# Performance work log

Measured on AMD Instinct MI355X. Metric: run time of the kernel, lower is better.

The kernel has to match this reference:

```python
import jax, jax.numpy as jnp
import numpy as np

N, D, M, K = 4096, 512, 50000, 32
TEMP = 0.1          # config.temperature
LAMBDA_GEOM = 0.1   # config.lambda_geom
LAMBDA_COMP = 0.1   # config.lambda_comp


def _unit(v):
    return v / jnp.linalg.norm(v, axis=-1, keepdims=True)


def setup_inputs() -> dict:
    key = jax.random.key(0)
    kx, km, ka, kk, kw, kb = jax.random.split(key, 6)
    x = _unit(jax.random.normal(kx, (N, D), jnp.float32))
    mu = _unit(jax.random.normal(km, (M, D), jnp.float32))            # splat directions
    alpha = jax.random.uniform(ka, (M,), jnp.float32, 1.0, 20.0)      # concentrations
    kappa = jax.random.uniform(kk, (M,), jnp.float32, 0.0, 2.0)       # importances
    W_w = jax.random.normal(kw, (3,), jnp.float32) * 0.5              # Linear(3,1) weight
    W_b = jax.random.normal(kb, (), jnp.float32) * 0.1                # Linear(3,1) bias
    return {"x": x, "mu": mu, "alpha": alpha, "kappa": kappa, "W_w": W_w, "W_b": W_b}


def reference(x, mu, alpha, kappa, W_w, W_b):
    # --- kNN over splats (find_neighbors): cosine/dot similarity top-k ---
    sims = x @ mu.T                                   # [N, M]
    dots, idx = jax.lax.top_k(sims, K)                # [N, K] neighbor dot-products + indices

    # --- splat energy: weighted logsumexp over neighbors ---
    n_alpha = alpha[idx]                              # [N, K]
    n_kappa = kappa[idx]                              # [N, K]
    imp = jnp.clip(n_kappa, 1e-4)
    weights = imp / imp.sum(axis=-1, keepdims=True)
    exponent = n_alpha * (dots - 1.0) / TEMP
    weighted = exponent + jnp.log(jnp.clip(weights, 1e-8))
    e_splat = -jax.nn.logsumexp(weighted, axis=-1)    # [N]

    # --- geom energy: off-diagonal pairwise spread ---
    S = x @ x.T                                       # [N, N]
    term = -jnp.log(1.0 - jnp.minimum(S, 1.0 - 1e-4) + 1e-4)
    n = x.shape[0]
    off = 1.0 - jnp.eye(n, dtype=S.dtype)
    e_geom = (term * off).sum() / (n * (n - 1))       # scalar: mean over off-diagonal

    # --- comp energy: top-2 neighbor dots through Linear(3,1) + sigmoid ---
    u = dots[:, 0]
    v = dots[:, 1]
    uv = jnp.stack([u, v, u * v], axis=-1)            # [N, 3]
    e_comp = jax.nn.sigmoid(uv @ W_w + W_b)           # [N]

    return e_splat + LAMBDA_GEOM * e_geom + LAMBDA_COMP * e_comp
```

## Files before the change

### kernel.cpp

```cpp
#include <hip/hip_runtime.h>
#include <math.h>

#define NR 4096
#define DD 512
#define MM 50000
#define CAP 640
#define TK 64
#define T0 0.118f
#define QS 400.0f
#define QINV (1.0f / 160000.0f)

typedef unsigned int u32;
typedef unsigned short u16;
typedef int i32x4 __attribute__((ext_vector_type(4)));

#define AS1 __attribute__((address_space(1)))
#define AS3 __attribute__((address_space(3)))

__device__ __forceinline__ u16 f2bf(float f) {
    u32 u = __float_as_uint(f);
    u32 r = (u + 0x7FFFu + ((u >> 16) & 1u)) >> 16;
    return (u16)r;
}


__global__ __launch_bounds__(256) void k_quant(const float* __restrict__ src,
                                               char* __restrict__ dst, int n8) {
    int i = blockIdx.x * 256 + threadIdx.x;
    if (i >= n8) return;
    const float4* s4 = (const float4*)src;
    float4 a = s4[(size_t)i * 2], b = s4[(size_t)i * 2 + 1];
    float v[8] = {a.x, a.y, a.z, a.w, b.x, b.y, b.z, b.w};
    u32 lo = 0, hi = 0;
#pragma unroll
    for (int j = 0; j < 4; ++j) {
        int q = __float2int_rn(v[j] * QS);
        q = q > 127 ? 127 : (q < -127 ? -127 : q);
        lo |= ((u32)(unsigned char)(char)q) << (8 * j);
    }
#pragma unroll
    for (int j = 0; j < 4; ++j) {
        int q = __float2int_rn(v[4 + j] * QS);
        q = q > 127 ? 127 : (q < -127 ? -127 : q);
        hi |= ((u32)(unsigned char)(char)q) << (8 * j);
    }
    *(uint2*)(dst + (size_t)i * 8) = make_uint2(lo, hi);
}

__global__ __launch_bounds__(256, 5) void k_gemm_topk(
    const char* __restrict__ xi8, const char* __restrict__ mui8,
    u32* __restrict__ cnt, u32* __restrict__ cand)
{
    __shared__ char smem[32768];

    const int t = threadIdx.x;
    const int lane = t & 63;
    const int wid = t >> 6;
    const int wr = wid >> 1, wc = wid & 1;
    const int fr = lane & 15, fq = lane >> 4;

    const u32 d   = (u32)blockIdx.y * (u32)gridDim.x + (u32)blockIdx.x;
    const u32 xcd = d & 7u;
    const u32 p   = xcd * 1564u + (d >> 3);
    const int r0  = (int)(p & 31u) * 128;
    const int c0  = (int)(p >> 5) * 128;

    i32x4 acc[4][4];
#pragma unroll
    for (int m = 0; m < 4; ++m)
#pragma unroll
        for (int n = 0; n < 4; ++n) acc[m][n] = (i32x4){0, 0, 0, 0};

    for (int kt = 0; kt < DD; kt += 128) {
        __syncthreads();
#pragma unroll
        for (int i = 0; i < 4; ++i) {
            const int L  = i * 4096 + t * 16;
            const int rw = L >> 7;
            const int cb = (L & 127) ^ ((rw & 7) << 4);
            const char* srcA = xi8 + (size_t)(r0 + rw) * DD + kt + cb;
            __builtin_amdgcn_global_load_lds((const AS1 u32*)srcA, (AS3 u32*)(smem + L), 16, 0, 0);
            int gr = c0 + rw; if (gr > MM - 1) gr = MM - 1;
            const char* srcB = mui8 + (size_t)gr * DD + kt + cb;
            __builtin_amdgcn_global_load_lds((const AS1 u32*)srcB, (AS3 u32*)(smem + 16384 + L), 16, 0, 0);
        }
        __syncthreads();
#pragma unroll
        for (int kk = 0; kk < 2; ++kk) {
            i32x4 af[4], bfr[4];
#pragma unroll
            for (int m = 0; m < 4; ++m) {
                const int ra = wr * 64 + m * 16 + fr;
                af[m] = *(const i32x4*)(smem + ((ra << 7) | ((kk * 64 + fq * 16) ^ ((ra & 7) << 4))));
            }
#pragma unroll
            for (int n = 0; n < 4; ++n) {
                const int rb = wc * 64 + n * 16 + fr;
                bfr[n] = *(const i32x4*)(smem + 16384 + ((rb << 7) | ((kk * 64 + fq * 16) ^ ((rb & 7) << 4))));
            }
#pragma unroll
            for (int m = 0; m < 4; ++m)
#pragma unroll
                for (int n = 0; n < 4; ++n)
                    acc[m][n] = __builtin_amdgcn_mfma_i32_16x16x64_i8(af[m], bfr[n], acc[m][n], 0, 0, 0);
        }
    }

#pragma unroll
    for (int m = 0; m < 4; ++m) {
        const int rowb = r0 + wr * 64 + m * 16 + fq * 4;
#pragma unroll
        for (int n = 0; n < 4; ++n) {
            const int col = c0 + wc * 64 + n * 16 + fr;
#pragma unroll
            for (int r = 0; r < 4; ++r) {
                const float v = (float)acc[m][n][r] * QINV;
                if (v >= T0 && col < MM) {
                    u32 pos = atomicAdd(&cnt[rowb + r], 1u);
                    if (pos < CAP)
                        cand[(size_t)(rowb + r) * CAP + pos] =
                            (((u32)f2bf(v)) << 16) | (u32)col;
                }
            }
        }
    }
}

__global__ __launch_bounds__(256, 5) void k_geom(
    const char* __restrict__ xi8, float* __restrict__ partial)
{
    const int bx = blockIdx.x, by = blockIdx.y;
    const int t = threadIdx.x;
    if (bx < by) { if (t == 0) partial[by * 32 + bx] = 0.f; return; }

    __shared__ char smem[32768];
    __shared__ float red[4];

    const int lane = t & 63;
    const int wid = t >> 6;
    const int wr = wid >> 1, wc = wid & 1;
    const int fr = lane & 15, fq = lane >> 4;
    const int r0 = by * 128;
    const int c0 = bx * 128;

    i32x4 acc[4][4];
#pragma unroll
    for (int m = 0; m < 4; ++m)
#pragma unroll
        for (int n = 0; n < 4; ++n) acc[m][n] = (i32x4){0, 0, 0, 0};

    for (int kt = 0; kt < DD; kt += 128) {
        __syncthreads();
#pragma unroll
        for (int i = 0; i < 4; ++i) {
            const int L  = i * 4096 + t * 16;
            const int rw = L >> 7;
            const int cb = (L & 127) ^ ((rw & 7) << 4);
            const char* srcA = xi8 + (size_t)(r0 + rw) * DD + kt + cb;
            __builtin_amdgcn_global_load_lds((const AS1 u32*)srcA, (AS3 u32*)(smem + L), 16, 0, 0);
            const char* srcB = xi8 + (size_t)(c0 + rw) * DD + kt + cb;
            __builtin_amdgcn_global_load_lds((const AS1 u32*)srcB, (AS3 u32*)(smem + 16384 + L), 16, 0, 0);
        }
        __syncthreads();
#pragma unroll
        for (int kk = 0; kk < 2; ++kk) {
            i32x4 af[4], bfr[4];
#pragma unroll
            for (int m = 0; m < 4; ++m) {
                const int ra = wr * 64 + m * 16 + fr;
                af[m] = *(const i32x4*)(smem + ((ra << 7) | ((kk * 64 + fq * 16) ^ ((ra & 7) << 4))));
            }
#pragma unroll
            for (int n = 0; n < 4; ++n) {
                const int rb = wc * 64 + n * 16 + fr;
                bfr[n] = *(const i32x4*)(smem + 16384 + ((rb << 7) | ((kk * 64 + fq * 16) ^ ((rb & 7) << 4))));
            }
#pragma unroll
            for (int m = 0; m < 4; ++m)
#pragma unroll
                for (int n = 0; n < 4; ++n)
                    acc[m][n] = __builtin_amdgcn_mfma_i32_16x16x64_i8(af[m], bfr[n], acc[m][n], 0, 0, 0);
        }
    }

    float local = 0.f;
#pragma unroll
    for (int m = 0; m < 4; ++m) {
        const int rowb = r0 + wr * 64 + m * 16 + fq * 4;
#pragma unroll
        for (int n = 0; n < 4; ++n) {
            const int col = c0 + wc * 64 + n * 16 + fr;
#pragma unroll
            for (int r = 0; r < 4; ++r) {
                if (rowb + r != col) {
                    float s = fminf((float)acc[m][n][r] * QINV, 0.9999f);
                    local += -logf(1.0f - s + 1e-4f);
                }
            }
        }
    }
    if (bx > by) local *= 2.f;

#pragma unroll
    for (int off = 32; off >= 1; off >>= 1) local += __shfl_xor(local, off, 64);
    if (lane == 0) red[wid] = local;
    __syncthreads();
    if (t == 0) partial[by * 32 + bx] = red[0] + red[1] + red[2] + red[3];
}

__global__ void k_reduce_geom(const float* __restrict__ partial, float* __restrict__ egeom)
{
    __shared__ float red[16];
    const int t = threadIdx.x;
    float v = partial[t];
#pragma unroll
    for (int off = 32; off >= 1; off >>= 1) v += __shfl_xor(v, off, 64);
    const int wave = t >> 6, lane = t & 63;
    if (lane == 0) red[wave] = v;
    __syncthreads();
    if (t == 0) {
        float s = 0.f;
        for (int i = 0; i < 16; ++i) s += red[i];
        egeom[0] = s / ((float)NR * (float)(NR - 1));
    }
}

__global__ __launch_bounds__(64) void k_finalize(
    const u32* __restrict__ cand, const u32* __restrict__ cnt,
    const float* __restrict__ x, const float* __restrict__ mu,
    const float* __restrict__ alpha, const float* __restrict__ kappa,
    const float* __restrict__ Ww, const float* __restrict__ Wb,
    const float* __restrict__ egeom, float* __restrict__ out)
{
    __shared__ u32   keys[CAP];
    __shared__ int   selid[TK];
    __shared__ float selex[TK];

    const int lane = threadIdx.x;
    const int row = blockIdx.x;
    const int cn = (int)cnt[row];
    const int c = cn < CAP ? cn : CAP;

    for (int s = lane; s < c; s += 64)
        keys[s] = cand[(size_t)row * CAP + s];
    __syncthreads();

    for (int k = 0; k < TK; ++k) {
        u32 best = 0u; int bpos = -1;
        for (int s = lane; s < c; s += 64) {
            u32 v = keys[s];
            if (v > best) { best = v; bpos = s; }
        }
#pragma unroll
        for (int off = 32; off >= 1; off >>= 1) {
            u32 v2 = __shfl_xor(best, off, 64);
            int p2 = __shfl_xor(bpos, off, 64);
            if (v2 > best) { best = v2; bpos = p2; }
        }
        if (lane == 0) {
            selid[k] = (bpos >= 0) ? (int)(best & 0xFFFFu) : -1;
            if (bpos >= 0) keys[bpos] = 0u;
        }
        __syncthreads();
    }

    float xr[8];
    {
        const float4* xp = (const float4*)(x + (size_t)row * DD);
        float4 a = xp[lane * 2], b = xp[lane * 2 + 1];
        xr[0] = a.x; xr[1] = a.y; xr[2] = a.z; xr[3] = a.w;
        xr[4] = b.x; xr[5] = b.y; xr[6] = b.z; xr[7] = b.w;
    }
    for (int s0 = 0; s0 < TK; s0 += 4) {
        int idv[4];
        float4 a0[4], a1[4];
#pragma unroll
        for (int j = 0; j < 4; ++j) {
            idv[j] = selid[s0 + j];
            const int rid = idv[j] >= 0 ? idv[j] : 0;
            const float4* mp = (const float4*)(mu + (size_t)rid * DD);
            a0[j] = mp[lane * 2];
            a1[j] = mp[lane * 2 + 1];
        }
        float d[4];
#pragma unroll
        for (int j = 0; j < 4; ++j)
            d[j] = xr[0] * a0[j].x + xr[1] * a0[j].y + xr[2] * a0[j].z + xr[3] * a0[j].w
                 + xr[4] * a1[j].x + xr[5] * a1[j].y + xr[6] * a1[j].z + xr[7] * a1[j].w;
#pragma unroll
        for (int j = 0; j < 4; ++j) {
#pragma unroll
            for (int off = 32; off >= 1; off >>= 1) d[j] += __shfl_xor(d[j], off, 64);
            if (lane == 0) selex[s0 + j] = (idv[j] >= 0) ? d[j] : -INFINITY;
        }
    }
    __syncthreads();

    float v = selex[lane];
    const int id = selid[lane];
    bool alive = (id >= 0);

    for (int rdrop = 0; rdrop < 32; ++rdrop) {
        float mn = alive ? v : INFINITY;
        int  mp2 = alive ? lane : 64;
#pragma unroll
        for (int off = 32; off >= 1; off >>= 1) {
            float m2 = __shfl_xor(mn, off, 64);
            int   p2 = __shfl_xor(mp2, off, 64);
            if (m2 < mn || (m2 == mn && p2 < mp2)) { mn = m2; mp2 = p2; }
        }
        if (lane == mp2) alive = false;
    }

    const float dv = alive ? v : -INFINITY;

    float m1 = dv; int p1 = alive ? lane : 64;
#pragma unroll
    for (int off = 32; off >= 1; off >>= 1) {
        float m2 = __shfl_xor(m1, off, 64);
        int   p2 = __shfl_xor(p1, off, 64);
        if (m2 > m1 || (m2 == m1 && p2 < p1)) { m1 = m2; p1 = p2; }
    }
    const float uu = m1;
    float s1 = (lane == p1) ? -INFINITY : dv;
#pragma unroll
    for (int off = 32; off >= 1; off >>= 1) s1 = fmaxf(s1, __shfl_xor(s1, off, 64));
    const float vv = s1;

    const int gid = alive ? id : 0;
    const float av = alpha[gid];
    const float kv = kappa[gid];
    float imp = alive ? fmaxf(kv, 1e-4f) : 0.f;
    float simp = imp;
#pragma unroll
    for (int off = 32; off >= 1; off >>= 1) simp += __shfl_xor(simp, off, 64);
    float w = fmaxf(imp / simp, 1e-8f);
    float tk = alive ? (av * (dv - 1.0f) * 10.0f + logf(w)) : -INFINITY;
    float mx = tk;
#pragma unroll
    for (int off = 32; off >= 1; off >>= 1) mx = fmaxf(mx, __shfl_xor(mx, off, 64));
    float se = alive ? expf(tk - mx) : 0.f;
#pragma unroll
    for (int off = 32; off >= 1; off >>= 1) se += __shfl_xor(se, off, 64);

    if (lane == 0) {
        float esplat = -(mx + logf(se));
        float z = Ww[0] * uu + Ww[1] * vv + Ww[2] * uu * vv + Wb[0];
        float ecomp = 1.f / (1.f + expf(-z));
        out[row] = esplat + 0.1f * egeom[0] + 0.1f * ecomp;
    }
}

extern "C" void kernel_launch(void* const* d_in, const int* in_sizes, int n_in,
                              void* d_out, int out_size, void* d_ws, size_t ws_size,
                              hipStream_t stream)
{
    const float* x     = (const float*)d_in[0];
    const float* mu    = (const float*)d_in[1];
    const float* alpha = (const float*)d_in[2];
    const float* kappa = (const float*)d_in[3];
    const float* Ww    = (const float*)d_in[4];
    const float* Wb    = (const float*)d_in[5];
    float* out = (float*)d_out;

    char* ws = (char*)d_ws;
    u32*   cnt     = (u32*)ws;
    float* partial = (float*)(ws + 16384);
    float* egeom   = (float*)(ws + 32768);
    char*  xi8     = (char*)(ws + 65536);
    char*  mui8    = (char*)(ws + 65536 + 2097152);
    u32*   cand    = (u32*)(ws + 65536 + 2097152 + 25600000);

    hipMemsetAsync(cnt, 0, NR * sizeof(u32), stream);

    k_quant<<<(NR * DD / 8 + 255) / 256, 256, 0, stream>>>(x, xi8, NR * DD / 8);
    k_quant<<<(MM * DD / 8 + 255) / 256, 256, 0, stream>>>(mu, mui8, MM * DD / 8);

    dim3 g1(NR / 128, (MM + 127) / 128);
    k_gemm_topk<<<g1, 256, 0, stream>>>(xi8, mui8, cnt, cand);

    dim3 g2(32, 32);
    k_geom<<<g2, 256, 0, stream>>>(xi8, partial);

    k_reduce_geom<<<1, 1024, 0, stream>>>(partial, egeom);

    k_finalize<<<NR, 64, 0, stream>>>(cand, cnt, x, mu, alpha, kappa, Ww, Wb, egeom, out);
}
```

Measured before the change: 449.2 us.

## Shard candidate counters per XCD group to cut cross-die atomic contention

Replaces the single per-row candidate counter and buffer with eight per-group slots, one per XCD-mapped block group, each capped at 64 entries. The finalize kernel gathers the eight sub-lists into shared memory. This targets contention and cross-die coherence traffic on global atomics in the GEMM epilogue. The threshold is also raised so fewer candidates are emitted. Both changes add a risk of losing true top-32 neighbours if one group overflows its cap or the stricter threshold leaves fewer than K candidates.

```diff
diff --git a/kernel.cpp b/kernel.cpp
--- a/kernel.cpp
+++ b/kernel.cpp
@@ -4,9 +4,9 @@
 #define NR 4096
 #define DD 512
 #define MM 50000
-#define CAP 640
+#define RCAP 64
 #define TK 64
-#define T0 0.118f
+#define T0 0.127f
 #define QS 400.0f
 #define QINV (1.0f / 160000.0f)
 
@@ -49,7 +49,7 @@
 
 __global__ __launch_bounds__(256, 5) void k_gemm_topk(
     const char* __restrict__ xi8, const char* __restrict__ mui8,
-    u32* __restrict__ cnt, u32* __restrict__ cand)
+    u32* __restrict__ cnt2, u32* __restrict__ cand2)
 {
     __shared__ char smem[32768];
 
@@ -60,8 +60,8 @@
     const int fr = lane & 15, fq = lane >> 4;
 
     const u32 d   = (u32)blockIdx.y * (u32)gridDim.x + (u32)blockIdx.x;
-    const u32 xcd = d & 7u;
-    const u32 p   = xcd * 1564u + (d >> 3);
+    const u32 g   = d & 7u;
+    const u32 p   = g * 1564u + (d >> 3);
     const int r0  = (int)(p & 31u) * 128;
     const int c0  = (int)(p >> 5) * 128;
 
@@ -116,9 +116,10 @@
             for (int r = 0; r < 4; ++r) {
                 const float v = (float)acc[m][n][r] * QINV;
                 if (v >= T0 && col < MM) {
-                    u32 pos = atomicAdd(&cnt[rowb + r], 1u);
-                    if (pos < CAP)
-                        cand[(size_t)(rowb + r) * CAP + pos] =
+                    const u32 slot = g * NR + (u32)(rowb + r);
+                    u32 pos = atomicAdd(&cnt2[slot], 1u);
+                    if (pos < RCAP)
+                        cand2[(size_t)slot * RCAP + pos] =
                             (((u32)f2bf(v)) << 16) | (u32)col;
                 }
             }
@@ -226,23 +227,30 @@
 }
 
 __global__ __launch_bounds__(64) void k_finalize(
-    const u32* __restrict__ cand, const u32* __restrict__ cnt,
+    const u32* __restrict__ cand2, const u32* __restrict__ cnt2,
     const float* __restrict__ x, const float* __restrict__ mu,
     const float* __restrict__ alpha, const float* __restrict__ kappa,
     const float* __restrict__ Ww, const float* __restrict__ Wb,
     const float* __restrict__ egeom, float* __restrict__ out)
 {
-    __shared__ u32   keys[CAP];
+    __shared__ u32   keys[8 * RCAP];
     __shared__ int   selid[TK];
     __shared__ float selex[TK];
 
     const int lane = threadIdx.x;
     const int row = blockIdx.x;
-    const int cn = (int)cnt[row];
-    const int c = cn < CAP ? cn : CAP;
-
-    for (int s = lane; s < c; s += 64)
-        keys[s] = cand[(size_t)row * CAP + s];
+
+    int total = 0;
+#pragma unroll
+    for (int g = 0; g < 8; ++g) {
+        const u32 slot = (u32)g * NR + (u32)row;
+        int cg = (int)cnt2[slot];
+        if (cg > RCAP) cg = RCAP;
+        if (lane < cg)
+            keys[total + lane] = cand2[(size_t)slot * RCAP + lane];
+        total += cg;
+    }
+    const int c = total;
     __syncthreads();
 
     for (int k = 0; k < TK; ++k) {
@@ -364,25 +372,25 @@
     float* out = (float*)d_out;
 
     char* ws = (char*)d_ws;
-    u32*   cnt     = (u32*)ws;
-    float* partial = (float*)(ws + 16384);
-    float* egeom   = (float*)(ws + 32768);
-    char*  xi8     = (char*)(ws + 65536);
-    char*  mui8    = (char*)(ws + 65536 + 2097152);
-    u32*   cand    = (u32*)(ws + 65536 + 2097152 + 25600000);
-
-    hipMemsetAsync(cnt, 0, NR * sizeof(u32), stream);
+    u32*   cnt2    = (u32*)ws;
+    float* partial = (float*)(ws + 131072);
+    float* egeom   = (float*)(ws + 135168);
+    char*  xi8     = (char*)(ws + 262144);
+    char*  mui8    = (char*)(ws + 262144 + 2097152);
+    u32*   cand2   = (u32*)(ws + 262144 + 2097152 + 25600000);
+
+    hipMemsetAsync(cnt2, 0, 8 * NR * sizeof(u32), stream);
 
     k_quant<<<(NR * DD / 8 + 255) / 256, 256, 0, stream>>>(x, xi8, NR * DD / 8);
     k_quant<<<(MM * DD / 8 + 255) / 256, 256, 0, stream>>>(mu, mui8, MM * DD / 8);
 
     dim3 g1(NR / 128, (MM + 127) / 128);
-    k_gemm_topk<<<g1, 256, 0, stream>>>(xi8, mui8, cnt, cand);
+    k_gemm_topk<<<g1, 256, 0, stream>>>(xi8, mui8, cnt2, cand2);
 
     dim3 g2(32, 32);
     k_geom<<<g2, 256, 0, stream>>>(xi8, partial);
 
     k_reduce_geom<<<1, 1024, 0, stream>>>(partial, egeom);
 
-    k_finalize<<<NR, 64, 0, stream>>>(cand, cnt, x, mu, alpha, kappa, Ww, Wb, egeom, out);
-}
+    k_finalize<<<NR, 64, 0, stream>>>(cand2, cnt2, x, mu, alpha, kappa, Ww, Wb, egeom, out);
+}
```

After: 414.5 us. -7.7%, faster.

## Replace global per-row candidate atomics with LDS counters and per-panel slots

Applied to the files above, without the earlier changes.

Candidate collection in the GEMM epilogue now counts per row in LDS and writes the first few hits into fixed per-(row, column-panel) slots. Only overflow goes through global atomics into a small overflow buffer. Finalize scans all panel slots, compacting the nonzero keys, and then the overflow list. This is meant to remove contended global atomics, but it adds a roughly 25 MB memset and a larger scan in finalize. The threshold is also raised slightly, which shrinks the candidate set.

```diff
diff --git a/kernel.cpp b/kernel.cpp
--- a/kernel.cpp
+++ b/kernel.cpp
@@ -4,9 +4,11 @@
 #define NR 4096
 #define DD 512
 #define MM 50000
-#define CAP 640
+#define NPAN 391
+#define DCAP 4
+#define OCAP 64
 #define TK 64
-#define T0 0.118f
+#define T0 0.120f
 #define QS 400.0f
 #define QINV (1.0f / 160000.0f)
 
@@ -49,7 +51,7 @@
 
 __global__ __launch_bounds__(256, 5) void k_gemm_topk(
     const char* __restrict__ xi8, const char* __restrict__ mui8,
-    u32* __restrict__ cnt, u32* __restrict__ cand)
+    u32* __restrict__ candD, u32* __restrict__ cntO, u32* __restrict__ candO)
 {
     __shared__ char smem[32768];
 
@@ -60,8 +62,8 @@
     const int fr = lane & 15, fq = lane >> 4;
 
     const u32 d   = (u32)blockIdx.y * (u32)gridDim.x + (u32)blockIdx.x;
-    const u32 xcd = d & 7u;
-    const u32 p   = xcd * 1564u + (d >> 3);
+    const u32 g   = d & 7u;
+    const u32 p   = g * 1564u + (d >> 3);
     const int r0  = (int)(p & 31u) * 128;
     const int c0  = (int)(p >> 5) * 128;
 
@@ -106,9 +108,15 @@
         }
     }
 
+    __syncthreads();
+    u32* ldsCnt = (u32*)smem;
+    if (t < 128) ldsCnt[t] = 0;
+    __syncthreads();
+
+    const int j = (int)(p >> 5);
 #pragma unroll
     for (int m = 0; m < 4; ++m) {
-        const int rowb = r0 + wr * 64 + m * 16 + fq * 4;
+        const int lr0 = wr * 64 + m * 16 + fq * 4;
 #pragma unroll
         for (int n = 0; n < 4; ++n) {
             const int col = c0 + wc * 64 + n * 16 + fr;
@@ -116,10 +124,15 @@
             for (int r = 0; r < 4; ++r) {
                 const float v = (float)acc[m][n][r] * QINV;
                 if (v >= T0 && col < MM) {
-                    u32 pos = atomicAdd(&cnt[rowb + r], 1u);
-                    if (pos < CAP)
-                        cand[(size_t)(rowb + r) * CAP + pos] =
-                            (((u32)f2bf(v)) << 16) | (u32)col;
+                    const int lrow = lr0 + r;
+                    u32 pos = atomicAdd(&ldsCnt[lrow], 1u);
+                    const u32 key = (((u32)f2bf(v)) << 16) | (u32)col;
+                    if (pos < DCAP) {
+                        candD[((size_t)(r0 + lrow) * NPAN + j) * DCAP + pos] = key;
+                    } else {
+                        u32 p2 = atomicAdd(&cntO[r0 + lrow], 1u);
+                        if (p2 < OCAP) candO[(size_t)(r0 + lrow) * OCAP + p2] = key;
+                    }
                 }
             }
         }
@@ -226,24 +239,38 @@
 }
 
 __global__ __launch_bounds__(64) void k_finalize(
-    const u32* __restrict__ cand, const u32* __restrict__ cnt,
+    const u32* __restrict__ candD, const u32* __restrict__ cntO,
+    const u32* __restrict__ candO,
     const float* __restrict__ x, const float* __restrict__ mu,
     const float* __restrict__ alpha, const float* __restrict__ kappa,
     const float* __restrict__ Ww, const float* __restrict__ Wb,
     const float* __restrict__ egeom, float* __restrict__ out)
 {
-    __shared__ u32   keys[CAP];
+    __shared__ u32   keys[512];
+    __shared__ u32   kc;
     __shared__ int   selid[TK];
     __shared__ float selex[TK];
 
     const int lane = threadIdx.x;
     const int row = blockIdx.x;
-    const int cn = (int)cnt[row];
-    const int c = cn < CAP ? cn : CAP;
-
-    for (int s = lane; s < c; s += 64)
-        keys[s] = cand[(size_t)row * CAP + s];
-    __syncthreads();
+
+    if (lane == 0) kc = 0;
+    __syncthreads();
+
+    const u32* rowD = candD + (size_t)row * NPAN * DCAP;
+    for (int s = lane; s < NPAN * DCAP; s += 64) {
+        u32 k = rowD[s];
+        if (k) { u32 q = atomicAdd(&kc, 1u); if (q < 512) keys[q] = k; }
+    }
+    {
+        int co = (int)cntO[row]; if (co > OCAP) co = OCAP;
+        for (int s = lane; s < co; s += 64) {
+            u32 k = candO[(size_t)row * OCAP + s];
+            u32 q = atomicAdd(&kc, 1u); if (q < 512) keys[q] = k;
+        }
+    }
+    __syncthreads();
+    int c = (int)kc; if (c > 512) c = 512;
 
     for (int k = 0; k < TK; ++k) {
         u32 best = 0u; int bpos = -1;
@@ -364,25 +391,27 @@
     float* out = (float*)d_out;
 
     char* ws = (char*)d_ws;
-    u32*   cnt     = (u32*)ws;
+    u32*   cntO    = (u32*)ws;
     float* partial = (float*)(ws + 16384);
-    float* egeom   = (float*)(ws + 32768);
-    char*  xi8     = (char*)(ws + 65536);
-    char*  mui8    = (char*)(ws + 65536 + 2097152);
-    u32*   cand    = (u32*)(ws + 65536 + 2097152 + 25600000);
-
-    hipMemsetAsync(cnt, 0, NR * sizeof(u32), stream);
+    float* egeom   = (float*)(ws + 20480);
+    char*  xi8     = (char*)(ws + 32768);
+    char*  mui8    = (char*)(ws + 32768 + 2097152);
+    u32*   candD   = (u32*)(ws + 32768 + 2097152 + 25600000);
+    u32*   candO   = (u32*)(ws + 32768 + 2097152 + 25600000 + 25624576);
+
+    hipMemsetAsync(cntO, 0, NR * sizeof(u32), stream);
+    hipMemsetAsync(candD, 0, (size_t)NR * NPAN * DCAP * sizeof(u32), stream);
 
     k_quant<<<(NR * DD / 8 + 255) / 256, 256, 0, stream>>>(x, xi8, NR * DD / 8);
     k_quant<<<(MM * DD / 8 + 255) / 256, 256, 0, stream>>>(mu, mui8, MM * DD / 8);
 
     dim3 g1(NR / 128, (MM + 127) / 128);
-    k_gemm_topk<<<g1, 256, 0, stream>>>(xi8, mui8, cnt, cand);
+    k_gemm_topk<<<g1, 256, 0, stream>>>(xi8, mui8, candD, cntO, candO);
 
     dim3 g2(32, 32);
     k_geom<<<g2, 256, 0, stream>>>(xi8, partial);
 
     k_reduce_geom<<<1, 1024, 0, stream>>>(partial, egeom);
 
-    k_finalize<<<NR, 64, 0, stream>>>(cand, cnt, x, mu, alpha, kappa, Ww, Wb, egeom, out);
-}
+    k_finalize<<<NR, 64, 0, stream>>>(candD, cntO, candO, x, mu, alpha, kappa, Ww, Wb, egeom, out);
+}
```

After: 460.7 us. 1.03x slower.
